# Kernel tuning notes

Measured on AMD Instinct MI355X. Metric: run time of the kernel, lower is better.

## Reference

```python
import jax, jax.numpy as jnp
import numpy as np

D_MODEL = 512
NUM_HEADS = 8
DEPTH = D_MODEL // NUM_HEADS
BATCH = 2
SEQ = 2048
NEG_INF_SCALE = -1e9


def setup_inputs() -> dict:
    key = jax.random.key(0)
    ks = jax.random.split(key, 9)
    s = 0.02
    return {
        "v": jax.random.normal(ks[0], (BATCH, SEQ, D_MODEL), jnp.float32),
        "q": jax.random.normal(ks[1], (BATCH, SEQ, D_MODEL), jnp.float32),
        "k": jax.random.normal(ks[2], (BATCH, SEQ, D_MODEL), jnp.float32),
        "mask": jax.random.randint(ks[3], (BATCH, 1, SEQ, SEQ), 0, 2, jnp.int32),
        "wq_w": jax.random.normal(ks[4], (D_MODEL, D_MODEL), jnp.float32) * s,
        "wq_b": jnp.zeros((D_MODEL,), jnp.float32),
        "wk_w": jax.random.normal(ks[5], (D_MODEL, D_MODEL), jnp.float32) * s,
        "wk_b": jnp.zeros((D_MODEL,), jnp.float32),
        "wv_w": jax.random.normal(ks[6], (D_MODEL, D_MODEL), jnp.float32) * s,
        "wv_b": jnp.zeros((D_MODEL,), jnp.float32),
        "wo_w": jax.random.normal(ks[7], (D_MODEL, D_MODEL), jnp.float32) * s,
        "wo_b": jnp.zeros((D_MODEL,), jnp.float32),
    }


def _split_heads(x, b):
    # [b, s, d_model] -> [b, h, s, depth]
    return x.reshape(b, -1, NUM_HEADS, DEPTH).transpose(0, 2, 1, 3)


def reference(v, q, k, mask, wq_w, wq_b, wk_w, wk_b, wv_w, wv_b, wo_w, wo_b):
    b = q.shape[0]
    vv = _split_heads(v @ wv_w + wv_b, b)  # [b,h,s,d]
    kk = _split_heads(k @ wk_w + wk_b, b)
    qq = _split_heads(q @ wq_w + wq_b, b)
    # NOTE: the original code swaps q/k at the helper call site, so logits = K @ Q^T.
    logits = jnp.einsum("bhkd,bhqd->bhkq", kk, qq) / jnp.sqrt(jnp.float32(DEPTH))
    logits = logits + mask.astype(jnp.float32) * NEG_INF_SCALE
    attn = jax.nn.softmax(logits, axis=-1)  # softmax over the query axis (faithful quirk)
    # output = A^T @ V  -> [b,h,q,d]
    out = jnp.einsum("bhkq,bhkd->bhqd", attn, vv)
    concat = out.transpose(0, 2, 1, 3).reshape(b, -1, D_MODEL)
    return concat @ wo_w + wo_b, attn
```

## Files before the change

kernel.cpp:

```cpp
#include <hip/hip_runtime.h>

#define S 2048
#define DM 512
#define NH 8
#define HD 64
#define NB 2
#define BH (NB * NH)
#define MROWS (NB * S)
#define QW (S / 32)

typedef __bf16 bf16x8 __attribute__((ext_vector_type(8)));
typedef float f32x4 __attribute__((ext_vector_type(4)));
typedef float nf4 __attribute__((ext_vector_type(4)));
typedef int ni4 __attribute__((ext_vector_type(4)));

#define QSCALE 0.18033688011112042f

__device__ __forceinline__ float hw_exp2(float x) {
  return __builtin_amdgcn_exp2f(x);
}

union FragU {
  uint4 u;
  bf16x8 v;
  unsigned short s[8];
};

__device__ __forceinline__ unsigned short f2bf(float x) {
  unsigned u = __float_as_uint(x);
  u += 0x7FFFu + ((u >> 16) & 1u);
  return (unsigned short)(u >> 16);
}

__global__ __launch_bounds__(256) void k_prep(
    const float* __restrict__ w0, const float* __restrict__ w1,
    const float* __restrict__ w2, const float* __restrict__ w3,
    unsigned short* __restrict__ wt,
    const float* __restrict__ q, const float* __restrict__ k, const float* __restrict__ v,
    unsigned short* __restrict__ oq, unsigned short* __restrict__ ok, unsigned short* __restrict__ ov,
    const int* __restrict__ mask, unsigned* __restrict__ mp,
    float* __restrict__ Zs) {
  __shared__ float tile[64][65];
  int bid = blockIdx.x;
  int tid = threadIdx.x;
  if (bid < 256) {
    int i = bid >> 6, rem = bid & 63;
    const float* w = (i == 0) ? w0 : (i == 1) ? w1 : (i == 2) ? w2 : w3;
    int k0 = (rem & 7) * 64, n0 = (rem >> 3) * 64;
    int tx = tid & 63, ty = tid >> 6;
    for (int r = ty; r < 64; r += 4)
      tile[r][tx] = w[(size_t)(k0 + r) * DM + n0 + tx];
    __syncthreads();
    unsigned short* o = wt + (size_t)i * DM * DM;
    for (int r = ty; r < 64; r += 4)
      o[(size_t)(n0 + r) * DM + k0 + tx] = f2bf(tile[tx][r]);
  } else if (bid < 3328) {
    int b2 = bid - 256;
    int which = b2 >> 10;
    const float* src = (which == 0) ? q : (which == 1) ? k : v;
    unsigned short* dst = (which == 0) ? oq : (which == 1) ? ok : ov;
    size_t t = (size_t)(b2 & 1023) * 256 + tid;
    const nf4* s4 = (const nf4*)src + t * 2;
    nf4 x = __builtin_nontemporal_load(s4);
    nf4 y = __builtin_nontemporal_load(s4 + 1);
    FragU f;
    f.s[0] = f2bf(x.x); f.s[1] = f2bf(x.y); f.s[2] = f2bf(x.z); f.s[3] = f2bf(x.w);
    f.s[4] = f2bf(y.x); f.s[5] = f2bf(y.y); f.s[6] = f2bf(y.z); f.s[7] = f2bf(y.w);
    *(uint4*)(dst + t * 8) = f.u;
  } else if (bid < 4352) {
    size_t t = (size_t)(bid - 3328) * 256 + tid;
    const ni4* mb = (const ni4*)(mask + t * 32);
    unsigned bits = 0;
#pragma unroll
    for (int c = 0; c < 8; c++) {
      ni4 m = __builtin_nontemporal_load(mb + c);
      bits |= (m.x != 0 ? 1u : 0u) << (c * 4);
      bits |= (m.y != 0 ? 1u : 0u) << (c * 4 + 1);
      bits |= (m.z != 0 ? 1u : 0u) << (c * 4 + 2);
      bits |= (m.w != 0 ? 1u : 0u) << (c * 4 + 3);
    }
    mp[t] = bits;
  } else {
    int t = (bid - 4352) * 256 + tid;
    ((float4*)Zs)[t] = make_float4(0.f, 0.f, 0.f, 0.f);
  }
}

__global__ __launch_bounds__(256) void k_proj(
    const unsigned short* __restrict__ inq, const unsigned short* __restrict__ ink,
    const unsigned short* __restrict__ inv, const unsigned short* __restrict__ wt,
    const float* __restrict__ bq, const float* __restrict__ bk, const float* __restrict__ bv,
    unsigned short* __restrict__ oq, unsigned short* __restrict__ ok,
    unsigned short* __restrict__ vvT) {
  __shared__ __align__(16) unsigned short vt[64][72];
  int which = blockIdx.z;
  const unsigned short* in = (which == 0) ? inq : (which == 1) ? ink : inv;
  const float* bias = (which == 0) ? bq : (which == 1) ? bk : bv;
  const unsigned short* w = wt + (size_t)which * DM * DM;

  int lane = threadIdx.x & 63, wv = threadIdx.x >> 6;
  int m0 = blockIdx.x * 64 + wv * 16;
  int n0 = blockIdx.y * 64;
  int kf = (lane >> 4) * 8;
  int arow = m0 + (lane & 15);

  f32x4 acc[4] = {{0.f, 0.f, 0.f, 0.f}, {0.f, 0.f, 0.f, 0.f},
                  {0.f, 0.f, 0.f, 0.f}, {0.f, 0.f, 0.f, 0.f}};

  for (int kk0 = 0; kk0 < DM; kk0 += 32) {
    FragU af;
    af.u = *(const uint4*)(in + (size_t)arow * DM + kk0 + kf);
#pragma unroll
    for (int nt = 0; nt < 4; nt++) {
      FragU bfr;
      bfr.u = *(const uint4*)(w + (size_t)(n0 + nt * 16 + (lane & 15)) * DM + kk0 + kf);
      acc[nt] = __builtin_amdgcn_mfma_f32_16x16x32_bf16(af.v, bfr.v, acc[nt], 0, 0, 0);
    }
  }

  if (which < 2) {
    unsigned short* out = (which == 0) ? oq : ok;
    float sc = (which == 0) ? QSCALE : 1.0f;
#pragma unroll
    for (int nt = 0; nt < 4; nt++) {
#pragma unroll
      for (int r = 0; r < 4; r++) {
        int row = m0 + (lane >> 4) * 4 + r;
        int col = n0 + nt * 16 + (lane & 15);
        float val = (acc[nt][r] + bias[col]) * sc;
        int b = row >> 11, sIdx = row & (S - 1);
        int h = col >> 6, d = col & 63;
        out[(((size_t)(b * NH + h) * S) + sIdx) * HD + d] = f2bf(val);
      }
    }
  } else {
#pragma unroll
    for (int nt = 0; nt < 4; nt++) {
#pragma unroll
      for (int r = 0; r < 4; r++) {
        int sl = wv * 16 + (lane >> 4) * 4 + r;
        int dl = nt * 16 + (lane & 15);
        vt[dl][sl] = f2bf(acc[nt][r] + bias[n0 + dl]);
      }
    }
    __syncthreads();
    int b = (blockIdx.x * 64) >> 11;
    int s0l = (blockIdx.x * 64) & (S - 1);
    int h = n0 >> 6;
    unsigned short* op = vvT + (size_t)(b * NH + h) * HD * S;
    int d = threadIdx.x >> 2;
    int sc2 = (threadIdx.x & 3) * 16;
#pragma unroll
    for (int j = 0; j < 2; j++)
      *(uint4*)&op[(size_t)d * S + s0l + sc2 + j * 8] = *(uint4*)&vt[d][sc2 + j * 8];
  }
}

__global__ __launch_bounds__(256, 4) void k_softmax_z(
    const unsigned short* __restrict__ qq, const unsigned short* __restrict__ kk,
    const unsigned* __restrict__ mp, float* __restrict__ Zsum) {
  int lane = threadIdx.x & 63, w = threadIdx.x >> 6;
  int bh = blockIdx.y;
  int b = bh >> 3;
  int k0 = blockIdx.x * 64 + w * 16;
  int kf = (lane >> 4) * 8;
  int qbase = blockIdx.z * (S / 2);
  int krow_b = k0 + (lane >> 4) * 4;

  const unsigned short* kbase = kk + ((size_t)bh * S + k0 + (lane & 15)) * HD + kf;
  FragU a0, a1;
  a0.u = *(const uint4*)kbase;
  a1.u = *(const uint4*)(kbase + 32);

  const unsigned short* qbaseP = qq + (size_t)bh * S * HD;
  const unsigned* mpb = mp + (size_t)b * S * QW;

  float sum[4] = {0.f, 0.f, 0.f, 0.f};

  for (int q0 = qbase; q0 < qbase + S / 2; q0 += 64) {
    uint2 mw[4];
#pragma unroll
    for (int r = 0; r < 4; r++)
      mw[r] = *(const uint2*)&mpb[(size_t)(krow_b + r) * QW + (q0 >> 5)];
#pragma unroll
    for (int nt = 0; nt < 4; nt++) {
      int qcol = q0 + nt * 16 + (lane & 15);
      const unsigned short* qp = qbaseP + (size_t)qcol * HD + kf;
      FragU b0, b1;
      b0.u = *(const uint4*)qp;
      b1.u = *(const uint4*)(qp + 32);
      f32x4 c = {0.f, 0.f, 0.f, 0.f};
      c = __builtin_amdgcn_mfma_f32_16x16x32_bf16(a0.v, b0.v, c, 0, 0, 0);
      c = __builtin_amdgcn_mfma_f32_16x16x32_bf16(a1.v, b1.v, c, 0, 0, 0);
      unsigned bpos = (unsigned)(nt * 16 + (lane & 15)) & 31u;
#pragma unroll
      for (int r = 0; r < 4; r++) {
        unsigned word = (nt < 2) ? mw[r].x : mw[r].y;
        float e = hw_exp2(c[r]);
        sum[r] += ((word >> bpos) & 1u) ? 0.f : e;
      }
    }
  }
#pragma unroll
  for (int r = 0; r < 4; r++) {
    float s = sum[r];
    s += __shfl_xor(s, 1);
    s += __shfl_xor(s, 2);
    s += __shfl_xor(s, 4);
    s += __shfl_xor(s, 8);
    if ((lane & 15) == 0)
      atomicAdd(&Zsum[(size_t)bh * S + krow_b + r], s);
  }
}

__global__ __launch_bounds__(512, 4) void k_attn(
    const unsigned short* __restrict__ qq, const unsigned short* __restrict__ kk,
    const unsigned short* __restrict__ vvT, const unsigned* __restrict__ mp,
    const float* __restrict__ Zsum, float* __restrict__ attn_out,
    unsigned short* __restrict__ conc) {
  __shared__ __align__(16) unsigned short pT[2][2][64][72];
  int lane = threadIdx.x & 63, w = threadIdx.x >> 6;
  int g = w >> 2, w4 = w & 3;
  int bh = blockIdx.y;
  int b = bh >> 3, h = bh & 7;
  int q0 = blockIdx.x * 64;
  int kf = (lane >> 4) * 8;

  FragU bq[4][2];
#pragma unroll
  for (int nt = 0; nt < 4; nt++) {
    const unsigned short* qp = qq + ((size_t)bh * S + q0 + nt * 16 + (lane & 15)) * HD + kf;
    bq[nt][0].u = *(const uint4*)qp;
    bq[nt][1].u = *(const uint4*)(qp + 32);
  }

  f32x4 o[4] = {{0.f, 0.f, 0.f, 0.f}, {0.f, 0.f, 0.f, 0.f},
                {0.f, 0.f, 0.f, 0.f}, {0.f, 0.f, 0.f, 0.f}};

  const unsigned short* kkb = kk + (size_t)bh * S * HD;
  const unsigned short* vb = vvT + (size_t)bh * HD * S;
  const unsigned* mpb = mp + (size_t)b * S * QW;
  float* ao = attn_out + (size_t)bh * S * S;
  const float* zb = Zsum + (size_t)bh * S;
  int q0w = q0 >> 5;
  int kbase = g * (S / 2);

  int buf = 0;
  for (int k0 = kbase; k0 < kbase + S / 2; k0 += 64) {
    int kw = k0 + w4 * 16;
    int krow_b = kw + (lane >> 4) * 4;
    const unsigned short* kp = kkb + (size_t)(kw + (lane & 15)) * HD + kf;
    FragU a0, a1;
    a0.u = *(const uint4*)kp;
    a1.u = *(const uint4*)(kp + 32);
    float iz[4];
    uint2 mw[4];
#pragma unroll
    for (int r = 0; r < 4; r++) {
      iz[r] = 1.0f / zb[krow_b + r];
      mw[r] = *(const uint2*)&mpb[(size_t)(krow_b + r) * QW + q0w];
    }

#pragma unroll
    for (int nt = 0; nt < 4; nt++) {
      f32x4 c = {0.f, 0.f, 0.f, 0.f};
      c = __builtin_amdgcn_mfma_f32_16x16x32_bf16(a0.v, bq[nt][0].v, c, 0, 0, 0);
      c = __builtin_amdgcn_mfma_f32_16x16x32_bf16(a1.v, bq[nt][1].v, c, 0, 0, 0);
      int ql = nt * 16 + (lane & 15);
      int qcol = q0 + ql;
      unsigned bpos = (unsigned)ql & 31u;
#pragma unroll
      for (int r = 0; r < 4; r++) {
        int kl = w4 * 16 + (lane >> 4) * 4 + r;
        int krow = k0 + kl;
        unsigned word = (nt < 2) ? mw[r].x : mw[r].y;
        float a = ((word >> bpos) & 1u) ? 0.f : hw_exp2(c[r]) * iz[r];
        __builtin_nontemporal_store(a, &ao[(size_t)krow * S + qcol]);
        pT[g][buf][ql][kl] = f2bf(a);
      }
    }
    __syncthreads();
#pragma unroll
    for (int ks = 0; ks < 2; ks++) {
      FragU af;
      af.u = *(const uint4*)(&pT[g][buf][w4 * 16 + (lane & 15)][kf + ks * 32]);
#pragma unroll
      for (int nt = 0; nt < 4; nt++) {
        FragU bfr;
        bfr.u = *(const uint4*)(vb + (size_t)(nt * 16 + (lane & 15)) * S + k0 + kf + ks * 32);
        o[nt] = __builtin_amdgcn_mfma_f32_16x16x32_bf16(af.v, bfr.v, o[nt], 0, 0, 0);
      }
    }
    buf ^= 1;
  }

  __syncthreads();
  float* oacc = (float*)&pT[0][0][0][0];
  int qr = w4 * 16 + (lane >> 4) * 4;
  if (g == 1) {
#pragma unroll
    for (int nt = 0; nt < 4; nt++)
#pragma unroll
      for (int r = 0; r < 4; r++)
        oacc[(qr + r) * 65 + nt * 16 + (lane & 15)] = o[nt][r];
  }
  __syncthreads();
  if (g == 0) {
#pragma unroll
    for (int nt = 0; nt < 4; nt++) {
#pragma unroll
      for (int r = 0; r < 4; r++) {
        int qg = q0 + qr + r;
        int col = h * 64 + nt * 16 + (lane & 15);
        float s = o[nt][r] + oacc[(qr + r) * 65 + nt * 16 + (lane & 15)];
        conc[((size_t)(b * S + qg)) * DM + col] = f2bf(s);
      }
    }
  }
}

__global__ __launch_bounds__(256) void k_outproj(
    const unsigned short* __restrict__ concat, const unsigned short* __restrict__ wt,
    const float* __restrict__ bias, float* __restrict__ out) {
  const unsigned short* w = wt + (size_t)3 * DM * DM;
  int lane = threadIdx.x & 63, wv = threadIdx.x >> 6;
  int m0 = blockIdx.x * 64 + wv * 16;
  int n0 = blockIdx.y * 64;
  int kf = (lane >> 4) * 8;

  f32x4 acc[4] = {{0.f, 0.f, 0.f, 0.f}, {0.f, 0.f, 0.f, 0.f},
                  {0.f, 0.f, 0.f, 0.f}, {0.f, 0.f, 0.f, 0.f}};

  for (int kk0 = 0; kk0 < DM; kk0 += 32) {
    FragU af;
    af.u = *(const uint4*)(concat + (size_t)(m0 + (lane & 15)) * DM + kk0 + kf);
#pragma unroll
    for (int nt = 0; nt < 4; nt++) {
      FragU bfr;
      bfr.u = *(const uint4*)(w + (size_t)(n0 + nt * 16 + (lane & 15)) * DM + kk0 + kf);
      acc[nt] = __builtin_amdgcn_mfma_f32_16x16x32_bf16(af.v, bfr.v, acc[nt], 0, 0, 0);
    }
  }
#pragma unroll
  for (int nt = 0; nt < 4; nt++) {
#pragma unroll
    for (int r = 0; r < 4; r++) {
      int row = m0 + (lane >> 4) * 4 + r;
      int col = n0 + nt * 16 + (lane & 15);
      out[(size_t)row * DM + col] = acc[nt][r] + bias[col];
    }
  }
}

extern "C" void kernel_launch(void* const* d_in, const int* in_sizes, int n_in,
                              void* d_out, int out_size, void* d_ws, size_t ws_size,
                              hipStream_t stream) {
  (void)in_sizes; (void)n_in; (void)out_size; (void)ws_size;
  const float* v    = (const float*)d_in[0];
  const float* q    = (const float*)d_in[1];
  const float* k    = (const float*)d_in[2];
  const int*   mask = (const int*)d_in[3];
  const float* wq_w = (const float*)d_in[4];
  const float* wq_b = (const float*)d_in[5];
  const float* wk_w = (const float*)d_in[6];
  const float* wk_b = (const float*)d_in[7];
  const float* wv_w = (const float*)d_in[8];
  const float* wv_b = (const float*)d_in[9];
  const float* wo_w = (const float*)d_in[10];
  const float* wo_b = (const float*)d_in[11];

  char* ws = (char*)d_ws;
  size_t off = 0;
  auto alloc = [&](size_t bytes) {
    char* p = ws + off;
    off += (bytes + 255) & ~(size_t)255;
    return p;
  };
  unsigned short* wt   = (unsigned short*)alloc((size_t)4 * DM * DM * 2);
  unsigned short* qbf  = (unsigned short*)alloc((size_t)MROWS * DM * 2);
  unsigned short* kbf  = (unsigned short*)alloc((size_t)MROWS * DM * 2);
  unsigned short* vbf  = (unsigned short*)alloc((size_t)MROWS * DM * 2);
  unsigned short* qq   = (unsigned short*)alloc((size_t)BH * S * HD * 2);
  unsigned short* kk2  = (unsigned short*)alloc((size_t)BH * S * HD * 2);
  unsigned short* vvT  = (unsigned short*)alloc((size_t)BH * S * HD * 2);
  unsigned*       mp   = (unsigned*)alloc((size_t)NB * S * QW * 4);
  float*          Zs   = (float*)alloc((size_t)BH * S * 4);
  unsigned short* conc = (unsigned short*)alloc((size_t)MROWS * DM * 2);

  float* out_final = (float*)d_out;
  float* out_attn  = (float*)d_out + (size_t)MROWS * DM;

  k_prep<<<dim3(4384), 256, 0, stream>>>(wq_w, wk_w, wv_w, wo_w, wt,
                                          q, k, v, qbf, kbf, vbf,
                                          mask, mp, Zs);
  k_proj<<<dim3(64, 8, 3), 256, 0, stream>>>(qbf, kbf, vbf, wt, wq_b, wk_b, wv_b,
                                              qq, kk2, vvT);
  k_softmax_z<<<dim3(32, 16, 2), 256, 0, stream>>>(qq, kk2, mp, Zs);
  k_attn<<<dim3(32, 16), 512, 0, stream>>>(qq, kk2, vvT, mp, Zs, out_attn, conc);
  k_outproj<<<dim3(64, 8), 256, 0, stream>>>(conc, wt, wo_b, out_final);
}
```

Before: 537.9 us.

## Stage Q tiles in LDS for row-sum kernel and replace atomics with partial sums

The softmax normaliser kernel now cooperatively loads each 64-row Q tile into a double-buffered shared-memory array, so the four waves share one global load instead of each fetching the same Q rows. The atomicAdd accumulation into Zsum is replaced by plain stores of two per-half partial sums, which the attention kernel adds before taking the reciprocal. This also removes the zero-initialisation blocks from the prep kernel. The cost is extra LDS use, a __syncthreads per iteration, and a second Z load in the attention loop.

```diff
diff --git a/kernel.cpp b/kernel.cpp
--- a/kernel.cpp
+++ b/kernel.cpp
@@ -38,8 +38,7 @@
     unsigned short* __restrict__ wt,
     const float* __restrict__ q, const float* __restrict__ k, const float* __restrict__ v,
     unsigned short* __restrict__ oq, unsigned short* __restrict__ ok, unsigned short* __restrict__ ov,
-    const int* __restrict__ mask, unsigned* __restrict__ mp,
-    float* __restrict__ Zs) {
+    const int* __restrict__ mask, unsigned* __restrict__ mp) {
   __shared__ float tile[64][65];
   int bid = blockIdx.x;
   int tid = threadIdx.x;
@@ -67,7 +66,7 @@
     f.s[0] = f2bf(x.x); f.s[1] = f2bf(x.y); f.s[2] = f2bf(x.z); f.s[3] = f2bf(x.w);
     f.s[4] = f2bf(y.x); f.s[5] = f2bf(y.y); f.s[6] = f2bf(y.z); f.s[7] = f2bf(y.w);
     *(uint4*)(dst + t * 8) = f.u;
-  } else if (bid < 4352) {
+  } else {
     size_t t = (size_t)(bid - 3328) * 256 + tid;
     const ni4* mb = (const ni4*)(mask + t * 32);
     unsigned bits = 0;
@@ -80,9 +79,6 @@
       bits |= (m.w != 0 ? 1u : 0u) << (c * 4 + 3);
     }
     mp[t] = bits;
-  } else {
-    int t = (bid - 4352) * 256 + tid;
-    ((float4*)Zs)[t] = make_float4(0.f, 0.f, 0.f, 0.f);
   }
 }
 
@@ -158,7 +154,8 @@
 
 __global__ __launch_bounds__(256, 4) void k_softmax_z(
     const unsigned short* __restrict__ qq, const unsigned short* __restrict__ kk,
-    const unsigned* __restrict__ mp, float* __restrict__ Zsum) {
+    const unsigned* __restrict__ mp, float* __restrict__ Zpart) {
+  __shared__ __align__(16) unsigned short qs[2][64][72];
   int lane = threadIdx.x & 63, w = threadIdx.x >> 6;
   int bh = blockIdx.y;
   int b = bh >> 3;
@@ -175,20 +172,34 @@
   const unsigned short* qbaseP = qq + (size_t)bh * S * HD;
   const unsigned* mpb = mp + (size_t)b * S * QW;
 
+  int sqr = threadIdx.x >> 2;
+  int sdc = (threadIdx.x & 3) * 16;
+
   float sum[4] = {0.f, 0.f, 0.f, 0.f};
 
+  {
+    const unsigned short* qp = qbaseP + (size_t)(qbase + sqr) * HD + sdc;
+    *(uint4*)&qs[0][sqr][sdc] = *(const uint4*)qp;
+    *(uint4*)&qs[0][sqr][sdc + 8] = *(const uint4*)(qp + 8);
+  }
+  __syncthreads();
+
+  int buf = 0;
   for (int q0 = qbase; q0 < qbase + S / 2; q0 += 64) {
+    if (q0 + 64 < qbase + S / 2) {
+      const unsigned short* qp = qbaseP + (size_t)(q0 + 64 + sqr) * HD + sdc;
+      *(uint4*)&qs[buf ^ 1][sqr][sdc] = *(const uint4*)qp;
+      *(uint4*)&qs[buf ^ 1][sqr][sdc + 8] = *(const uint4*)(qp + 8);
+    }
     uint2 mw[4];
 #pragma unroll
     for (int r = 0; r < 4; r++)
       mw[r] = *(const uint2*)&mpb[(size_t)(krow_b + r) * QW + (q0 >> 5)];
 #pragma unroll
     for (int nt = 0; nt < 4; nt++) {
-      int qcol = q0 + nt * 16 + (lane & 15);
-      const unsigned short* qp = qbaseP + (size_t)qcol * HD + kf;
       FragU b0, b1;
-      b0.u = *(const uint4*)qp;
-      b1.u = *(const uint4*)(qp + 32);
+      b0.u = *(const uint4*)&qs[buf][nt * 16 + (lane & 15)][kf];
+      b1.u = *(const uint4*)&qs[buf][nt * 16 + (lane & 15)][kf + 32];
       f32x4 c = {0.f, 0.f, 0.f, 0.f};
       c = __builtin_amdgcn_mfma_f32_16x16x32_bf16(a0.v, b0.v, c, 0, 0, 0);
       c = __builtin_amdgcn_mfma_f32_16x16x32_bf16(a1.v, b1.v, c, 0, 0, 0);
@@ -200,7 +211,10 @@
         sum[r] += ((word >> bpos) & 1u) ? 0.f : e;
       }
     }
-  }
+    __syncthreads();
+    buf ^= 1;
+  }
+  float* zp = Zpart + ((size_t)blockIdx.z * BH + bh) * S;
 #pragma unroll
   for (int r = 0; r < 4; r++) {
     float s = sum[r];
@@ -209,14 +223,14 @@
     s += __shfl_xor(s, 4);
     s += __shfl_xor(s, 8);
     if ((lane & 15) == 0)
-      atomicAdd(&Zsum[(size_t)bh * S + krow_b + r], s);
+      zp[krow_b + r] = s;
   }
 }
 
 __global__ __launch_bounds__(512, 4) void k_attn(
     const unsigned short* __restrict__ qq, const unsigned short* __restrict__ kk,
     const unsigned short* __restrict__ vvT, const unsigned* __restrict__ mp,
-    const float* __restrict__ Zsum, float* __restrict__ attn_out,
+    const float* __restrict__ Zpart, float* __restrict__ attn_out,
     unsigned short* __restrict__ conc) {
   __shared__ __align__(16) unsigned short pT[2][2][64][72];
   int lane = threadIdx.x & 63, w = threadIdx.x >> 6;
@@ -241,7 +255,8 @@
   const unsigned short* vb = vvT + (size_t)bh * HD * S;
   const unsigned* mpb = mp + (size_t)b * S * QW;
   float* ao = attn_out + (size_t)bh * S * S;
-  const float* zb = Zsum + (size_t)bh * S;
+  const float* zb0 = Zpart + (size_t)bh * S;
+  const float* zb1 = Zpart + (size_t)(BH + bh) * S;
   int q0w = q0 >> 5;
   int kbase = g * (S / 2);
 
@@ -257,7 +272,7 @@
     uint2 mw[4];
 #pragma unroll
     for (int r = 0; r < 4; r++) {
-      iz[r] = 1.0f / zb[krow_b + r];
+      iz[r] = 1.0f / (zb0[krow_b + r] + zb1[krow_b + r]);
       mw[r] = *(const uint2*)&mpb[(size_t)(krow_b + r) * QW + q0w];
     }
 
@@ -384,15 +399,15 @@
   unsigned short* kk2  = (unsigned short*)alloc((size_t)BH * S * HD * 2);
   unsigned short* vvT  = (unsigned short*)alloc((size_t)BH * S * HD * 2);
   unsigned*       mp   = (unsigned*)alloc((size_t)NB * S * QW * 4);
-  float*          Zs   = (float*)alloc((size_t)BH * S * 4);
+  float*          Zs   = (float*)alloc((size_t)2 * BH * S * 4);
   unsigned short* conc = (unsigned short*)alloc((size_t)MROWS * DM * 2);
 
   float* out_final = (float*)d_out;
   float* out_attn  = (float*)d_out + (size_t)MROWS * DM;
 
-  k_prep<<<dim3(4384), 256, 0, stream>>>(wq_w, wk_w, wv_w, wo_w, wt,
+  k_prep<<<dim3(4352), 256, 0, stream>>>(wq_w, wk_w, wv_w, wo_w, wt,
                                           q, k, v, qbf, kbf, vbf,
-                                          mask, mp, Zs);
+                                          mask, mp);
   k_proj<<<dim3(64, 8, 3), 256, 0, stream>>>(qbf, kbf, vbf, wt, wq_b, wk_b, wv_b,
                                               qq, kk2, vvT);
   k_softmax_z<<<dim3(32, 16, 2), 256, 0, stream>>>(qq, kk2, mp, Zs);
```

Measured after the change: 492.2 us. -8.5%, faster.
